# Optimization experiments

Measured on AMD Instinct MI355X. Metric: run time of the kernel, lower is better.

## Reference

```python
import jax, jax.numpy as jnp
import numpy as np

N_SRC = 100000   # source nodes
N_DST = 50000    # destination nodes
E = 600000       # edges (avg dst degree ~12)
D_IN = 128
D_OUT = 128


def setup_inputs() -> dict:
    key = jax.random.key(0)
    k1, k2, k3, k4 = jax.random.split(key, 4)
    H_src = jax.random.normal(k1, (N_SRC, D_IN), dtype=jnp.float32)
    edge_src = jax.random.randint(k2, (E,), 0, N_SRC)
    edge_dst = jax.random.randint(k3, (E,), 0, N_DST)
    # xavier_uniform-style scale for W
    limit = float(np.sqrt(6.0 / (D_IN + D_OUT)))
    W = jax.random.uniform(k4, (D_IN, D_OUT), dtype=jnp.float32, minval=-limit, maxval=limit)
    b = jnp.zeros((D_OUT,), dtype=jnp.float32)
    return {"H_src": H_src, "W": W, "b": b,
            "edge_src": edge_src, "edge_dst": edge_dst, "n_dst": N_DST}


def reference(H_src, W, b, edge_src, edge_dst, n_dst):
    # Linear transform: WH = H_src @ W + b        [N_src, D_OUT]
    WH = H_src @ W + b
    # Sparse aggregation: (A @ WH) as gather + segment_sum over edges
    agg = jax.ops.segment_sum(WH[edge_src], edge_dst, num_segments=n_dst)  # [N_dst, D_OUT]
    # Degree normalization: deg = row-sum of A, clamped to >= 1
    deg = jax.ops.segment_sum(jnp.ones(edge_dst.shape, WH.dtype), edge_dst,
                              num_segments=n_dst)
    deg = jnp.maximum(deg, 1.0)[:, None]
    return jax.nn.relu(agg / deg)
```

## Files before the change

### kernel.cpp

```cpp
#include <hip/hip_runtime.h>

#define D 128
#define LDA 136
#define BCAP 64
#define CSTRIDE 16
#define OVCAP 65536

typedef __attribute__((ext_vector_type(8))) short bf16x8;
typedef __attribute__((ext_vector_type(4))) float f32x4;
typedef __attribute__((ext_vector_type(4))) unsigned int u32x4;

static __device__ __forceinline__ unsigned short f2bf(float f) {
    unsigned u = __float_as_uint(f);
    unsigned r = 0x7fffu + ((u >> 16) & 1u);
    return (unsigned short)((u + r) >> 16);
}
static __device__ __forceinline__ float bflo(unsigned u) { return __uint_as_float(u << 16); }
static __device__ __forceinline__ float bfhi(unsigned u) { return __uint_as_float(u & 0xffff0000u); }

__global__ __launch_bounds__(256) void zero_wt_kernel(
    const float* __restrict__ W, unsigned short* __restrict__ Wt,
    int* __restrict__ counts, int nz4)
{
    int i = blockIdx.x * 256 + threadIdx.x;
    if (i < nz4) ((u32x4*)counts)[i] = (u32x4){0u, 0u, 0u, 0u};
    if (i < 8192) {
        int n = i >> 6, k2 = (i & 63) << 1;
        unsigned lo = f2bf(W[(size_t)k2 * 128 + n]);
        unsigned hi = f2bf(W[(size_t)(k2 + 1) * 128 + n]);
        ((unsigned*)Wt)[(size_t)n * 64 + (k2 >> 1)] = lo | (hi << 16);
    }
}

__global__ __launch_bounds__(256, 8) void prep_gemm_kernel(
    const float* __restrict__ H, int n_src,
    const unsigned short* __restrict__ Wt, unsigned short* __restrict__ WHb,
    const int* __restrict__ esrc, const int* __restrict__ edst, int E,
    int* __restrict__ counts, int* __restrict__ buckets,
    int* __restrict__ ovcnt, int* __restrict__ ovd, int* __restrict__ ovs)
{
    __shared__ __align__(16) unsigned short Wsh[64 * LDA];

    const int tid = threadIdx.x, bid = blockIdx.x;
    const int gt = (int)gridDim.x * 256;

    int e0 = bid * 256 + tid, e1 = e0 + gt;
    bool h0 = (e0 < E), h1 = (e1 < E);
    int d0 = 0, s0 = 0, d1 = 0, s1 = 0, c0 = 0, c1 = 0;
    if (h0) { d0 = __builtin_nontemporal_load(edst + e0);
              s0 = __builtin_nontemporal_load(esrc + e0); }
    if (h1) { d1 = __builtin_nontemporal_load(edst + e1);
              s1 = __builtin_nontemporal_load(esrc + e1); }
    if (h0) c0 = atomicAdd(&counts[(size_t)d0 * CSTRIDE], 1);
    if (h1) c1 = atomicAdd(&counts[(size_t)d1 * CSTRIDE], 1);

    const int lane = tid & 63, wvid = tid >> 6;
    const int fl = lane & 15, quad = lane >> 4;
    const int rowbase = bid * 64;
    const int m0 = wvid * 16;
    const bool doG = (rowbase < n_src);

#pragma unroll
    for (int t = 0; t < 4; ++t) {
        int i = tid + t * 256;
        int nn = i >> 4, k8 = (i & 15) << 3;
        *(uint4*)&Wsh[nn * LDA + k8] = ((const uint4*)Wt)[nn * 16 + (i & 15)];
    }

    int arow = rowbase + m0 + fl;
    bool rok = doG && (arow < n_src);
    const f32x4* H4 = (const f32x4*)H;
    size_t base = (size_t)(rok ? arow : 0) * 32 + quad * 2;
    f32x4 z = (f32x4){0.f, 0.f, 0.f, 0.f};
    f32x4 av0 = z, av1 = z, av2 = z, av3 = z, av4 = z, av5 = z, av6 = z, av7 = z;
    if (rok) {
        av0 = H4[base +  0]; av1 = H4[base +  1];
        av2 = H4[base +  8]; av3 = H4[base +  9];
        av4 = H4[base + 16]; av5 = H4[base + 17];
        av6 = H4[base + 24]; av7 = H4[base + 25];
    }
    __syncthreads();

    f32x4 cacc[8];
#pragma unroll
    for (int n = 0; n < 8; ++n) cacc[n] = (f32x4){0.f, 0.f, 0.f, 0.f};

#define PACK_A(a, v0, v1)                                                    \
    { a[0] = (short)f2bf(v0.x); a[1] = (short)f2bf(v0.y);                    \
      a[2] = (short)f2bf(v0.z); a[3] = (short)f2bf(v0.w);                    \
      a[4] = (short)f2bf(v1.x); a[5] = (short)f2bf(v1.y);                    \
      a[6] = (short)f2bf(v1.z); a[7] = (short)f2bf(v1.w); }
#define MSTEP(a, KC, NL, CI)                                                  \
    { bf16x8 bf = *(const bf16x8*)&Wsh[((NL) * 16 + fl) * LDA + (KC) + quad * 8]; \
      cacc[CI] = __builtin_amdgcn_mfma_f32_16x16x32_bf16(a, bf, cacc[CI], 0, 0, 0); }

    bf16x8 a0, a1, a2, a3;
    PACK_A(a0, av0, av1) PACK_A(a1, av2, av3)
    PACK_A(a2, av4, av5) PACK_A(a3, av6, av7)

    if (doG) {
#pragma unroll
        for (int nl = 0; nl < 4; ++nl) {
            MSTEP(a0, 0, nl, nl) MSTEP(a1, 32, nl, nl)
            MSTEP(a2, 64, nl, nl) MSTEP(a3, 96, nl, nl)
        }
    }
    __syncthreads();

#pragma unroll
    for (int t = 0; t < 4; ++t) {
        int i = tid + t * 256;
        int nn = i >> 4, k8 = (i & 15) << 3;
        *(uint4*)&Wsh[nn * LDA + k8] = ((const uint4*)Wt)[(64 + nn) * 16 + (i & 15)];
    }
    __syncthreads();

    if (doG) {
#pragma unroll
        for (int nl = 0; nl < 4; ++nl) {
            MSTEP(a0, 0, nl, nl + 4) MSTEP(a1, 32, nl, nl + 4)
            MSTEP(a2, 64, nl, nl + 4) MSTEP(a3, 96, nl, nl + 4)
        }
    }
    __syncthreads();
#undef PACK_A
#undef MSTEP

    if (doG) {
        unsigned short* Csh = Wsh;
#pragma unroll
        for (int n = 0; n < 8; ++n) {
            int col = n * 16 + fl;
#pragma unroll
            for (int r = 0; r < 4; ++r)
                Csh[(m0 + quad * 4 + r) * LDA + col] = f2bf(cacc[n][r]);
        }
#pragma unroll
        for (int t = 0; t < 4; ++t) {
            int c = lane + t * 64;
            int row = m0 + (c >> 4), chunk = c & 15;
            size_t gr = (size_t)rowbase + row;
            if (gr < (size_t)n_src) {
                u32x4 v = *(const u32x4*)&Csh[row * LDA + chunk * 8];
                ((u32x4*)WHb)[gr * 16 + chunk] = v;
            }
        }
    }

    if (h0) {
        if (c0 < BCAP) buckets[(size_t)d0 * BCAP + c0] = s0;
        else { int o = atomicAdd(ovcnt, 1); if (o < OVCAP) { ovd[o] = d0; ovs[o] = s0; } }
    }
    if (h1) {
        if (c1 < BCAP) buckets[(size_t)d1 * BCAP + c1] = s1;
        else { int o = atomicAdd(ovcnt, 1); if (o < OVCAP) { ovd[o] = d1; ovs[o] = s1; } }
    }
    for (int e = e0 + 2 * gt; e < E; e += gt) {
        int dd = edst[e], ss = esrc[e];
        int cc = atomicAdd(&counts[(size_t)dd * CSTRIDE], 1);
        if (cc < BCAP) buckets[(size_t)dd * BCAP + cc] = ss;
        else { int o = atomicAdd(ovcnt, 1); if (o < OVCAP) { ovd[o] = dd; ovs[o] = ss; } }
    }
}

__global__ __launch_bounds__(256) void agg_finalize_kernel(
    const uint4* __restrict__ WHb, const int* __restrict__ buckets,
    const int* __restrict__ counts, const int* __restrict__ ovcnt,
    const int* __restrict__ ovd, const int* __restrict__ ovs,
    const float* __restrict__ b, float* __restrict__ out, int n_dst)
{
    int dst = blockIdx.x * 4 + (threadIdx.x >> 6);
    if (dst >= n_dst) return;
    int lane = threadIdx.x & 63;
    int dg = __builtin_nontemporal_load(counts + (size_t)dst * CSTRIDE);
    int m = dg < BCAP ? dg : BCAP;
    int nov = *ovcnt; if (nov > OVCAP) nov = OVCAP;
    int idx = (lane < m)
        ? __builtin_nontemporal_load(buckets + (size_t)dst * BCAP + lane) : 0;

    const int ql = lane & 15, quad = lane >> 4;
    float acc[8] = {0, 0, 0, 0, 0, 0, 0, 0};

    if (m > 0) {
        int c0 = quad, c1 = quad + 4, c2 = quad + 8, c3 = quad + 12;
        int l0 = c0 < m ? c0 : m - 1;
        int l1 = c1 < m ? c1 : m - 1;
        int l2 = c2 < m ? c2 : m - 1;
        int l3 = c3 < m ? c3 : m - 1;
        int s0 = __shfl(idx, l0), s1 = __shfl(idx, l1);
        int s2 = __shfl(idx, l2), s3 = __shfl(idx, l3);
        uint4 h0 = WHb[(size_t)s0 * 16 + ql];
        uint4 h1 = WHb[(size_t)s1 * 16 + ql];
        uint4 h2 = WHb[(size_t)s2 * 16 + ql];
        uint4 h3 = WHb[(size_t)s3 * 16 + ql];
        float w0 = (c0 < m) ? 1.f : 0.f, w1 = (c1 < m) ? 1.f : 0.f;
        float w2 = (c2 < m) ? 1.f : 0.f, w3 = (c3 < m) ? 1.f : 0.f;
        acc[0] = w0*bflo(h0.x) + w1*bflo(h1.x) + w2*bflo(h2.x) + w3*bflo(h3.x);
        acc[1] = w0*bfhi(h0.x) + w1*bfhi(h1.x) + w2*bfhi(h2.x) + w3*bfhi(h3.x);
        acc[2] = w0*bflo(h0.y) + w1*bflo(h1.y) + w2*bflo(h2.y) + w3*bflo(h3.y);
        acc[3] = w0*bfhi(h0.y) + w1*bfhi(h1.y) + w2*bfhi(h2.y) + w3*bfhi(h3.y);
        acc[4] = w0*bflo(h0.z) + w1*bflo(h1.z) + w2*bflo(h2.z) + w3*bflo(h3.z);
        acc[5] = w0*bfhi(h0.z) + w1*bfhi(h1.z) + w2*bfhi(h2.z) + w3*bfhi(h3.z);
        acc[6] = w0*bflo(h0.w) + w1*bflo(h1.w) + w2*bflo(h2.w) + w3*bflo(h3.w);
        acc[7] = w0*bfhi(h0.w) + w1*bfhi(h1.w) + w2*bfhi(h2.w) + w3*bfhi(h3.w);
    }

    int j = 16;
    for (; j + 8 <= m; j += 8) {
        int sA = __shfl(idx, j + quad);
        int sB = __shfl(idx, j + 4 + quad);
        uint4 ha = WHb[(size_t)sA * 16 + ql];
        uint4 hb = WHb[(size_t)sB * 16 + ql];
        acc[0] += bflo(ha.x) + bflo(hb.x); acc[1] += bfhi(ha.x) + bfhi(hb.x);
        acc[2] += bflo(ha.y) + bflo(hb.y); acc[3] += bfhi(ha.y) + bfhi(hb.y);
        acc[4] += bflo(ha.z) + bflo(hb.z); acc[5] += bfhi(ha.z) + bfhi(hb.z);
        acc[6] += bflo(ha.w) + bflo(hb.w); acc[7] += bfhi(ha.w) + bfhi(hb.w);
    }
    for (; j < m; j += 4) {
        int jj = j + quad;
        int s = __shfl(idx, jj < m ? jj : m - 1);
        uint4 hv = WHb[(size_t)s * 16 + ql];
        float w = (jj < m) ? 1.f : 0.f;
        acc[0] += w * bflo(hv.x); acc[1] += w * bfhi(hv.x);
        acc[2] += w * bflo(hv.y); acc[3] += w * bfhi(hv.y);
        acc[4] += w * bflo(hv.z); acc[5] += w * bfhi(hv.z);
        acc[6] += w * bflo(hv.w); acc[7] += w * bfhi(hv.w);
    }
    for (int k = quad; k < nov; k += 4) {
        if (ovd[k] == dst) {
            uint4 hv = WHb[(size_t)ovs[k] * 16 + ql];
            acc[0] += bflo(hv.x); acc[1] += bfhi(hv.x);
            acc[2] += bflo(hv.y); acc[3] += bfhi(hv.y);
            acc[4] += bflo(hv.z); acc[5] += bfhi(hv.z);
            acc[6] += bflo(hv.w); acc[7] += bfhi(hv.w);
        }
    }
#pragma unroll
    for (int k = 0; k < 8; ++k) {
        acc[k] += __shfl_xor(acc[k], 16);
        acc[k] += __shfl_xor(acc[k], 32);
    }
    if (quad == 0) {
        float inv  = 1.0f / (float)(dg > 1 ? dg : 1);
        float gate = (dg > 0) ? 1.0f : 0.0f;
        const f32x4* b4 = (const f32x4*)b;
        f32x4 b0 = b4[ql * 2], b1 = b4[ql * 2 + 1];
        f32x4 o0, o1;
        o0.x = fmaxf(acc[0] * inv + b0.x * gate, 0.f);
        o0.y = fmaxf(acc[1] * inv + b0.y * gate, 0.f);
        o0.z = fmaxf(acc[2] * inv + b0.z * gate, 0.f);
        o0.w = fmaxf(acc[3] * inv + b0.w * gate, 0.f);
        o1.x = fmaxf(acc[4] * inv + b1.x * gate, 0.f);
        o1.y = fmaxf(acc[5] * inv + b1.y * gate, 0.f);
        o1.z = fmaxf(acc[6] * inv + b1.z * gate, 0.f);
        o1.w = fmaxf(acc[7] * inv + b1.w * gate, 0.f);
        f32x4* op = (f32x4*)out + (size_t)dst * 32 + ql * 2;
        __builtin_nontemporal_store(o0, op);
        __builtin_nontemporal_store(o1, op + 1);
    }
}

__global__ __launch_bounds__(256) void prep_fb_kernel(
    const int* __restrict__ esrc, const int* __restrict__ edst, int E,
    int* __restrict__ counts, int* __restrict__ buckets,
    int* __restrict__ ovcnt, int* __restrict__ ovd, int* __restrict__ ovs)
{
    int i = blockIdx.x * 256 + threadIdx.x;
    if (i >= E) return;
    int d = edst[i], s = esrc[i];
    int c = atomicAdd(&counts[(size_t)d * CSTRIDE], 1);
    if (c < BCAP) buckets[(size_t)d * BCAP + c] = s;
    else { int o = atomicAdd(ovcnt, 1); if (o < OVCAP) { ovd[o] = d; ovs[o] = s; } }
}

__global__ __launch_bounds__(256) void aggregate_kernel_f32(
    const float* __restrict__ H,
    const int* __restrict__ buckets, const int* __restrict__ counts,
    const int* __restrict__ ovcnt, const int* __restrict__ ovd,
    const int* __restrict__ ovs, unsigned short* __restrict__ aggb, int n_dst)
{
    int dst = blockIdx.x * 4 + (threadIdx.x >> 6);
    if (dst >= n_dst) return;
    int lane = threadIdx.x & 63;
    int dg = counts[(size_t)dst * CSTRIDE];
    int m = dg < BCAP ? dg : BCAP;
    int nov = *ovcnt; if (nov > OVCAP) nov = OVCAP;
    int idx = (lane < m) ? buckets[(size_t)dst * BCAP + lane] : 0;

    const int hl = lane & 31, half = lane >> 5;
    const float4* H4 = (const float4*)H;
    float acc[4] = {0, 0, 0, 0};
    int j = 0;
    for (; j + 4 <= m; j += 4) {
        int sA = __shfl(idx, j + half);
        int sB = __shfl(idx, j + 2 + half);
        float4 va = H4[(size_t)sA * 32 + hl];
        float4 vb = H4[(size_t)sB * 32 + hl];
        acc[0] += va.x + vb.x; acc[1] += va.y + vb.y;
        acc[2] += va.z + vb.z; acc[3] += va.w + vb.w;
    }
    for (; j < m; j += 2) {
        int jj = j + half;
        int s = __shfl(idx, jj < m ? jj : m - 1);
        float4 v = H4[(size_t)s * 32 + hl];
        float w = (jj < m) ? 1.f : 0.f;
        acc[0] += w * v.x; acc[1] += w * v.y;
        acc[2] += w * v.z; acc[3] += w * v.w;
    }
    for (int k = half; k < nov; k += 2) {
        if (ovd[k] == dst) {
            float4 v = H4[(size_t)ovs[k] * 32 + hl];
            acc[0] += v.x; acc[1] += v.y; acc[2] += v.z; acc[3] += v.w;
        }
    }
#pragma unroll
    for (int k = 0; k < 4; ++k) acc[k] += __shfl_xor(acc[k], 32);
    if (half == 0) {
        uint2 o;
        o.x = (unsigned)f2bf(acc[0]) | ((unsigned)f2bf(acc[1]) << 16);
        o.y = (unsigned)f2bf(acc[2]) | ((unsigned)f2bf(acc[3]) << 16);
        ((uint2*)aggb)[(size_t)dst * 32 + hl] = o;
    }
}

__global__ __launch_bounds__(256) void gemm_finalize_kernel(
    const unsigned short* __restrict__ aggb, const unsigned short* __restrict__ Wt,
    const float* __restrict__ b, const int* __restrict__ counts,
    float* __restrict__ out, int n_dst)
{
    __shared__ __align__(16) unsigned char smem[52224];
    unsigned short* Ash = (unsigned short*)smem;
    unsigned short* Wsh = (unsigned short*)(smem + 64 * LDA * 2);
    float* Csh = (float*)smem;

    const int tid  = threadIdx.x;
    const int lane = tid & 63, wv = tid >> 6;
    const size_t row0 = (size_t)blockIdx.x * 64;

#pragma unroll
    for (int t = 0; t < 4; ++t) {
        int i = tid + t * 256;
        int r = i >> 4, k8 = (i & 15) << 3;
        size_t gr = row0 + r;
        uint4 v = (gr < (size_t)n_dst) ? ((const uint4*)aggb)[gr * 16 + (i & 15)]
                                       : make_uint4(0, 0, 0, 0);
        *(uint4*)&Ash[r * LDA + k8] = v;
    }
#pragma unroll
    for (int t = 0; t < 8; ++t) {
        int i = tid + t * 256;
        int n = i >> 4, k8 = (i & 15) << 3;
        *(uint4*)&Wsh[n * LDA + k8] = ((const uint4*)Wt)[i];
    }
    __syncthreads();

    const int m0 = wv * 16;
    const int fl = lane & 15, quad = lane >> 4;

    f32x4 cacc[8];
#pragma unroll
    for (int n = 0; n < 8; ++n) cacc[n] = (f32x4){0.f, 0.f, 0.f, 0.f};

#pragma unroll
    for (int kc = 0; kc < 128; kc += 32) {
        bf16x8 a = *(const bf16x8*)&Ash[(m0 + fl) * LDA + kc + quad * 8];
#pragma unroll
        for (int n = 0; n < 8; ++n) {
            bf16x8 bf = *(const bf16x8*)&Wsh[(n * 16 + fl) * LDA + kc + quad * 8];
            cacc[n] = __builtin_amdgcn_mfma_f32_16x16x32_bf16(a, bf, cacc[n], 0, 0, 0);
        }
    }

    float inv[4], gate[4];
#pragma unroll
    for (int r = 0; r < 4; ++r) {
        size_t gr = row0 + m0 + quad * 4 + r;
        int dg = (gr < (size_t)n_dst) ? counts[gr * CSTRIDE] : 0;
        inv[r]  = 1.0f / (float)(dg > 1 ? dg : 1);
        gate[r] = (dg > 0) ? 1.0f : 0.0f;
    }
    __syncthreads();

#pragma unroll
    for (int n = 0; n < 8; ++n) {
        int col = n * 16 + fl;
        float bc = b[col];
#pragma unroll
        for (int r = 0; r < 4; ++r) {
            float v = cacc[n][r] * inv[r] + bc * gate[r];
            Csh[(m0 + quad * 4 + r) * 132 + col] = fmaxf(v, 0.0f);
        }
    }
    __syncthreads();

#pragma unroll
    for (int t = 0; t < 8; ++t) {
        int i = tid + t * 256;
        int rr = i >> 5, c4 = i & 31;
        size_t gr = row0 + rr;
        if (gr < (size_t)n_dst) {
            f32x4 vout = *(f32x4*)&Csh[rr * 132 + c4 * 4];
            __builtin_nontemporal_store(vout, (f32x4*)out + gr * (D / 4) + c4);
        }
    }
}

extern "C" void kernel_launch(void* const* d_in, const int* in_sizes, int n_in,
                              void* d_out, int out_size, void* d_ws, size_t ws_size,
                              hipStream_t stream) {
    const float* H    = (const float*)d_in[0];
    const float* W    = (const float*)d_in[1];
    const float* b    = (const float*)d_in[2];
    const int*   esrc = (const int*)d_in[3];
    const int*   edst = (const int*)d_in[4];
    const int    E     = in_sizes[3];
    const int    n_dst = out_size / D;
    const int    nsrc_elems = in_sizes[0];
    const int    n_src = nsrc_elems / D;

    float* out = (float*)d_out;

    char* p = (char*)d_ws;
    unsigned short* Wt = (unsigned short*)p;  p += 128 * 128 * sizeof(unsigned short);
    int* counts = (int*)p;  p += (size_t)n_dst * CSTRIDE * 4;
    int* ovcnt  = (int*)p;  p += 256;
    int* ovd    = (int*)p;  p += (size_t)OVCAP * 4;
    int* ovs    = (int*)p;  p += (size_t)OVCAP * 4;
    int* buckets= (int*)p;  p += (size_t)n_dst * BCAP * 4;
    size_t agg_off = (((size_t)(p - (char*)d_ws)) + 255) & ~(size_t)255;
    unsigned short* aggb = (unsigned short*)((char*)d_ws + agg_off);
    size_t wh_off = (agg_off + (size_t)n_dst * D * 2 + 255) & ~(size_t)255;
    bool use_wh = (ws_size >= wh_off + (size_t)nsrc_elems * 2);
    unsigned short* WHb = (unsigned short*)((char*)d_ws + wh_off);

    int nz4 = (n_dst * CSTRIDE + 64) / 4;
    int gz = nz4 > 8192 ? nz4 : 8192;
    zero_wt_kernel<<<(gz + 255) / 256, 256, 0, stream>>>(W, Wt, counts, nz4);

    if (use_wh) {
        int G = (n_src + 63) / 64;
        int Ge = (E + 511) / 512;
        if (Ge > G) G = Ge;
        prep_gemm_kernel<<<G, 256, 0, stream>>>(
            H, n_src, Wt, WHb, esrc, edst, E, counts, buckets, ovcnt, ovd, ovs);
        agg_finalize_kernel<<<(n_dst + 3) / 4, 256, 0, stream>>>(
            (const uint4*)WHb, buckets, counts, ovcnt, ovd, ovs, b, out, n_dst);
    } else {
        prep_fb_kernel<<<(E + 255) / 256, 256, 0, stream>>>(
            esrc, edst, E, counts, buckets, ovcnt, ovd, ovs);
        aggregate_kernel_f32<<<(n_dst + 3) / 4, 256, 0, stream>>>(
            H, buckets, counts, ovcnt, ovd, ovs, aggb, n_dst);
        gemm_finalize_kernel<<<(n_dst + 63) / 64, 256, 0, stream>>>(
            aggb, Wt, b, counts, out, n_dst);
    }
}
```

Baseline: 159.0 us.

## Replace global-atomic bucket fill with two-level radix binning of edges by destination

```diff
diff --git a/kernel.cpp b/kernel.cpp
--- a/kernel.cpp
+++ b/kernel.cpp
@@ -20,10 +20,11 @@
 
 __global__ __launch_bounds__(256) void zero_wt_kernel(
     const float* __restrict__ W, unsigned short* __restrict__ Wt,
-    int* __restrict__ counts, int nz4)
+    int* __restrict__ counts, int nz4, int* __restrict__ binctl, int nbz)
 {
     int i = blockIdx.x * 256 + threadIdx.x;
     if (i < nz4) ((u32x4*)counts)[i] = (u32x4){0u, 0u, 0u, 0u};
+    if (i < nbz) ((u32x4*)binctl)[i] = (u32x4){0u, 0u, 0u, 0u};
     if (i < 8192) {
         int n = i >> 6, k2 = (i & 63) << 1;
         unsigned lo = f2bf(W[(size_t)k2 * 128 + n]);
@@ -35,30 +36,29 @@
 __global__ __launch_bounds__(256, 8) void prep_gemm_kernel(
     const float* __restrict__ H, int n_src,
     const unsigned short* __restrict__ Wt, unsigned short* __restrict__ WHb,
-    const int* __restrict__ esrc, const int* __restrict__ edst, int E,
-    int* __restrict__ counts, int* __restrict__ buckets,
-    int* __restrict__ ovcnt, int* __restrict__ ovd, int* __restrict__ ovs)
+    const int* __restrict__ edst, int E, int* __restrict__ bincnt)
 {
     __shared__ __align__(16) unsigned short Wsh[64 * LDA];
+    __shared__ int hist[256];
 
     const int tid = threadIdx.x, bid = blockIdx.x;
-    const int gt = (int)gridDim.x * 256;
-
-    int e0 = bid * 256 + tid, e1 = e0 + gt;
-    bool h0 = (e0 < E), h1 = (e1 < E);
-    int d0 = 0, s0 = 0, d1 = 0, s1 = 0, c0 = 0, c1 = 0;
-    if (h0) { d0 = __builtin_nontemporal_load(edst + e0);
-              s0 = __builtin_nontemporal_load(esrc + e0); }
-    if (h1) { d1 = __builtin_nontemporal_load(edst + e1);
-              s1 = __builtin_nontemporal_load(esrc + e1); }
-    if (h0) c0 = atomicAdd(&counts[(size_t)d0 * CSTRIDE], 1);
-    if (h1) c1 = atomicAdd(&counts[(size_t)d1 * CSTRIDE], 1);
+
+    if (bid < 256) {
+        hist[tid] = 0;
+        __syncthreads();
+        for (int e = bid * 256 + tid; e < E; e += 65536)
+            atomicAdd(&hist[((unsigned)__builtin_nontemporal_load(edst + e)) >> 8], 1);
+        __syncthreads();
+        int v = hist[tid];
+        if (v) atomicAdd(&bincnt[tid], v);
+    }
 
     const int lane = tid & 63, wvid = tid >> 6;
     const int fl = lane & 15, quad = lane >> 4;
     const int rowbase = bid * 64;
     const int m0 = wvid * 16;
     const bool doG = (rowbase < n_src);
+    if (!doG) return;
 
 #pragma unroll
     for (int t = 0; t < 4; ++t) {
@@ -68,7 +68,7 @@
     }
 
     int arow = rowbase + m0 + fl;
-    bool rok = doG && (arow < n_src);
+    bool rok = (arow < n_src);
     const f32x4* H4 = (const f32x4*)H;
     size_t base = (size_t)(rok ? arow : 0) * 32 + quad * 2;
     f32x4 z = (f32x4){0.f, 0.f, 0.f, 0.f};
@@ -98,12 +98,10 @@
     PACK_A(a0, av0, av1) PACK_A(a1, av2, av3)
     PACK_A(a2, av4, av5) PACK_A(a3, av6, av7)
 
-    if (doG) {
-#pragma unroll
-        for (int nl = 0; nl < 4; ++nl) {
-            MSTEP(a0, 0, nl, nl) MSTEP(a1, 32, nl, nl)
-            MSTEP(a2, 64, nl, nl) MSTEP(a3, 96, nl, nl)
-        }
+#pragma unroll
+    for (int nl = 0; nl < 4; ++nl) {
+        MSTEP(a0, 0, nl, nl) MSTEP(a1, 32, nl, nl)
+        MSTEP(a2, 64, nl, nl) MSTEP(a3, 96, nl, nl)
     }
     __syncthreads();
 
@@ -115,18 +113,16 @@
     }
     __syncthreads();
 
-    if (doG) {
-#pragma unroll
-        for (int nl = 0; nl < 4; ++nl) {
-            MSTEP(a0, 0, nl, nl + 4) MSTEP(a1, 32, nl, nl + 4)
-            MSTEP(a2, 64, nl, nl + 4) MSTEP(a3, 96, nl, nl + 4)
-        }
+#pragma unroll
+    for (int nl = 0; nl < 4; ++nl) {
+        MSTEP(a0, 0, nl, nl + 4) MSTEP(a1, 32, nl, nl + 4)
+        MSTEP(a2, 64, nl, nl + 4) MSTEP(a3, 96, nl, nl + 4)
     }
     __syncthreads();
 #undef PACK_A
 #undef MSTEP
 
-    if (doG) {
+    {
         unsigned short* Csh = Wsh;
 #pragma unroll
         for (int n = 0; n < 8; ++n) {
@@ -146,20 +142,100 @@
             }
         }
     }
-
-    if (h0) {
-        if (c0 < BCAP) buckets[(size_t)d0 * BCAP + c0] = s0;
-        else { int o = atomicAdd(ovcnt, 1); if (o < OVCAP) { ovd[o] = d0; ovs[o] = s0; } }
-    }
-    if (h1) {
-        if (c1 < BCAP) buckets[(size_t)d1 * BCAP + c1] = s1;
-        else { int o = atomicAdd(ovcnt, 1); if (o < OVCAP) { ovd[o] = d1; ovs[o] = s1; } }
-    }
-    for (int e = e0 + 2 * gt; e < E; e += gt) {
-        int dd = edst[e], ss = esrc[e];
-        int cc = atomicAdd(&counts[(size_t)dd * CSTRIDE], 1);
-        if (cc < BCAP) buckets[(size_t)dd * BCAP + cc] = ss;
-        else { int o = atomicAdd(ovcnt, 1); if (o < OVCAP) { ovd[o] = dd; ovs[o] = ss; } }
+}
+
+__global__ __launch_bounds__(256) void scatter_kernel(
+    const int* __restrict__ esrc, const int* __restrict__ edst, int E,
+    const int* __restrict__ bincnt, int* __restrict__ bincur,
+    int2* __restrict__ binbuf)
+{
+    __shared__ int sh_d[2048];
+    __shared__ int sh_s[2048];
+    __shared__ int hist[256];
+    __shared__ int sc[256];
+    __shared__ int base[256];
+
+    const int tid = threadIdx.x, bid = blockIdx.x;
+    const int e0 = bid * 2048;
+
+    hist[tid] = 0;
+    __syncthreads();
+#pragma unroll
+    for (int t = 0; t < 8; ++t) {
+        int i = t * 256 + tid, e = e0 + i;
+        if (e < E) {
+            int d = __builtin_nontemporal_load(edst + e);
+            int s = __builtin_nontemporal_load(esrc + e);
+            sh_d[i] = d; sh_s[i] = s;
+            atomicAdd(&hist[(unsigned)d >> 8], 1);
+        }
+    }
+    int bc = bincnt[tid];
+    sc[tid] = bc;
+    __syncthreads();
+    for (int off = 1; off < 256; off <<= 1) {
+        int v = (tid >= off) ? sc[tid - off] : 0;
+        __syncthreads();
+        sc[tid] += v;
+        __syncthreads();
+    }
+    int h = hist[tid];
+    base[tid] = (sc[tid] - bc) + (h ? atomicAdd(&bincur[tid], h) : 0);
+    hist[tid] = 0;
+    __syncthreads();
+#pragma unroll
+    for (int t = 0; t < 8; ++t) {
+        int i = t * 256 + tid, e = e0 + i;
+        if (e < E) {
+            int d = sh_d[i];
+            int r = atomicAdd(&hist[(unsigned)d >> 8], 1);
+            binbuf[base[(unsigned)d >> 8] + r] = make_int2(sh_s[i], d);
+        }
+    }
+}
+
+__global__ __launch_bounds__(256) void fine_kernel(
+    const int2* __restrict__ binbuf, const int* __restrict__ bincnt,
+    int* __restrict__ counts, int* __restrict__ buckets,
+    int* __restrict__ ovcnt, int* __restrict__ ovd, int* __restrict__ ovs,
+    int n_dst)
+{
+    __shared__ int sc[256];
+    __shared__ int hist[256];
+    __shared__ int sse[2];
+
+    const int tid = threadIdx.x, bin = blockIdx.x;
+
+    int bc = bincnt[tid];
+    sc[tid] = bc;
+    hist[tid] = 0;
+    __syncthreads();
+    for (int off = 1; off < 256; off <<= 1) {
+        int v = (tid >= off) ? sc[tid - off] : 0;
+        __syncthreads();
+        sc[tid] += v;
+        __syncthreads();
+    }
+    if (tid == bin) { sse[0] = sc[tid] - bc; sse[1] = bc; }
+    __syncthreads();
+    const int start = sse[0], cnt = sse[1];
+
+    for (int i = tid; i < cnt; i += 256) {
+        int2 es = binbuf[start + i];
+        atomicAdd(&hist[es.y & 255], 1);
+    }
+    __syncthreads();
+    int deg = hist[tid];
+    int d = (bin << 8) + tid;
+    if (d < n_dst) counts[(size_t)d * CSTRIDE] = deg;
+    __syncthreads();
+    hist[tid] = 0;
+    __syncthreads();
+    for (int i = tid; i < cnt; i += 256) {
+        int2 es = binbuf[start + i];
+        int r = atomicAdd(&hist[es.y & 255], 1);
+        if (r < BCAP) buckets[(size_t)es.y * BCAP + r] = es.x;
+        else { int o = atomicAdd(ovcnt, 1); if (o < OVCAP) { ovd[o] = es.y; ovs[o] = es.x; } }
     }
 }
 
@@ -430,19 +506,32 @@
     size_t agg_off = (((size_t)(p - (char*)d_ws)) + 255) & ~(size_t)255;
     unsigned short* aggb = (unsigned short*)((char*)d_ws + agg_off);
     size_t wh_off = (agg_off + (size_t)n_dst * D * 2 + 255) & ~(size_t)255;
-    bool use_wh = (ws_size >= wh_off + (size_t)nsrc_elems * 2);
     unsigned short* WHb = (unsigned short*)((char*)d_ws + wh_off);
+    size_t bc_off = (wh_off + (size_t)nsrc_elems * 2 + 255) & ~(size_t)255;
+    int* bincnt = (int*)((char*)d_ws + bc_off);
+    int2* binbuf = (int2*)aggb;
+
+    bool use_wh = (ws_size >= bc_off + 2048)
+               && (n_dst <= 65536) && (n_dst > 0)
+               && ((size_t)E * 8 <= (size_t)n_dst * D * 2);
 
     int nz4 = (n_dst * CSTRIDE + 64) / 4;
     int gz = nz4 > 8192 ? nz4 : 8192;
-    zero_wt_kernel<<<(gz + 255) / 256, 256, 0, stream>>>(W, Wt, counts, nz4);
+    zero_wt_kernel<<<(gz + 255) / 256, 256, 0, stream>>>(
+        W, Wt, counts, nz4, use_wh ? bincnt : counts, use_wh ? 128 : 0);
 
     if (use_wh) {
         int G = (n_src + 63) / 64;
-        int Ge = (E + 511) / 512;
-        if (Ge > G) G = Ge;
+        if (G < 256) G = 256;
         prep_gemm_kernel<<<G, 256, 0, stream>>>(
-            H, n_src, Wt, WHb, esrc, edst, E, counts, buckets, ovcnt, ovd, ovs);
+            H, n_src, Wt, WHb, edst, E, bincnt);
+        int SG = (E + 2047) / 2048;
+        if (SG > 0)
+            scatter_kernel<<<SG, 256, 0, stream>>>(
+                esrc, edst, E, bincnt, bincnt + 256, binbuf);
+        int NB = (n_dst + 255) >> 8;
+        fine_kernel<<<NB, 256, 0, stream>>>(
+            binbuf, bincnt, counts, buckets, ovcnt, ovd, ovs, n_dst);
         agg_finalize_kernel<<<(n_dst + 3) / 4, 256, 0, stream>>>(
             (const uint4*)WHb, buckets, counts, ovcnt, ovd, ovs, b, out, n_dst);
     } else {
```

Measured after the change: 162.2 us. Within noise of the previous version (+2.0%).
